# Kernel tuning notes

Hardware: AMD Instinct MI355X
Metric: run time of the kernel (lower is better)

## Reference

```python
import jax, jax.numpy as jnp
import numpy as np


def _cost_volume(image, coords, psize, ksize):
    # image: [c, h, w]; coords: [num, 2] pixel centers; returns [num, psize*psize]
    c, h, w = image.shape
    sp = psize // 2
    pad = ksize // 2 + sp
    ipad = jnp.pad(image, ((0, 0), (pad, pad), (pad, pad)))
    ky = jnp.arange(ksize)
    # top-left corner (in padded coords, before search shift) of each center patch
    rows = coords[:, 0, None, None] + ky[None, :, None]   # [num, k, 1]
    cols = coords[:, 1, None, None] + ky[None, None, :]   # [num, 1, k]
    center = ipad[:, rows + sp, cols + sp]                # [c, num, k, k]
    offs = jnp.stack(jnp.meshgrid(jnp.arange(psize), jnp.arange(psize), indexing='ij'), -1).reshape(-1, 2)

    def ssd(d):
        shifted = ipad[:, rows + d[0], cols + d[1]]       # [c, num, k, k]
        return jnp.sum((shifted - center) ** 2, axis=(0, 2, 3))  # [num]

    vol = jax.lax.map(ssd, offs)                          # [psize*psize, num]
    return vol.T


def _sim_map(image, coords, sigma, psize, ksize):
    c = image.shape[0]
    q = _cost_volume(image, coords, psize, ksize) / (c * ksize * ksize)
    q = jnp.exp(-q / jax.nn.relu(sigma) + 1e-20)          # sigma: [1] broadcasts
    return q[None]                                        # [1, num, psize*psize]


def setup_inputs() -> dict:
    key = jax.random.key(0)
    k1, k2, k3 = jax.random.split(key, 3)
    H = W = 256
    C = 3
    NUM = 2048
    return {
        "img": jax.random.normal(k1, (1, C, H, W), jnp.float32),
        "img_sr": jax.random.normal(k2, (1, C, H, W), jnp.float32),
        "sigma": jnp.array([4.0], jnp.float32),
        "coords": jax.random.randint(k3, (NUM, 2), 0, H),
        "kernel_size_search": 25,
        "kernel_size_center": 9,
    }


def reference(img, img_sr, sigma, coords, kernel_size_search, kernel_size_center):
    s = _sim_map(img[0], coords, sigma, kernel_size_search, kernel_size_center)
    s1 = _sim_map(img_sr[0], coords, sigma, kernel_size_search, kernel_size_center)
    return (s, s1)
```

## Files before the change

kernel.cpp:

```cpp
#include <hip/hip_runtime.h>
#include <hip/hip_fp16.h>

typedef unsigned int uint;
typedef __attribute__((ext_vector_type(2))) _Float16 half2_t;

#define NUM 2048
#define SP 12
#define WIN 33
#define RSTR 20
#define WA_DW (3*WIN*RSTR)
#define HS_STRIDE 14
#define HSE_DW (2*WA_DW)
#define HSO_DW (HSE_DW + WIN*HS_STRIDE)
#define TOT_DW (HSO_DW + WIN*HS_STRIDE)
#define PARTS_DW WA_DW
#define PSTR 8

union U32H2 { uint u; half2_t h; };
__device__ __forceinline__ half2_t uh2(uint u){ U32H2 p; p.u=u; return p.h; }

#if __has_builtin(__builtin_amdgcn_fdot2)
__device__ __forceinline__ float fdot2(uint a, uint b, float c) {
    return __builtin_amdgcn_fdot2(uh2(a), uh2(b), c, false);
}
#else
__device__ __forceinline__ float fdot2(uint a, uint b, float c) {
    half2_t A = uh2(a), B = uh2(b);
    return fmaf((float)A.y, (float)B.y, fmaf((float)A.x, (float)B.x, c));
}
#endif

__device__ __forceinline__ uint packh2(float a, float b) {
    return (uint)__half_as_ushort(__float2half(a)) |
           ((uint)__half_as_ushort(__float2half(b)) << 16);
}

__global__ __launch_bounds__(256, 8) void simmap_kernel(
    const float* __restrict__ img, const float* __restrict__ img_sr,
    const float* __restrict__ sigma, const int* __restrict__ coords,
    float* __restrict__ out)
{
    __shared__ __align__(16) uint lds[TOT_DW];
    __half* wh = (__half*)lds;
    float*  lf = (float*)lds;

    const int n = blockIdx.x;
    const int imgid = blockIdx.y;
    const float* im = imgid ? img_sr : img;
    const int t = threadIdx.x;
    const int w = t >> 6;
    const int l = t & 63;
    const int r0 = coords[2*n];
    const int c0 = coords[2*n+1];

    if (r0 >= 16 && r0 < 240 && c0 >= 16 && c0 < 240) {
        const float* base = im + (r0-16)*256 + (c0-16);
        for (int f = t; f < WIN*WIN; f += 256) {
            int r = f / WIN, x = f - r*WIN;
            int go = r*256 + x;
            #pragma unroll
            for (int c = 0; c < 3; ++c) {
                __half hv = __float2half(base[c*65536 + go]);
                int rowh = (c*WIN + r)*40;
                wh[rowh + x] = hv;
                if (x >= 1)  wh[2*WA_DW + rowh + x - 1] = hv;
                if (x == 32) wh[rowh + 33] = __float2half(0.f);
            }
        }
    } else {
        for (int f = t; f < WIN*WIN; f += 256) {
            int r = f / WIN, x = f - r*WIN;
            int ri = r0 + r - 16, ci = c0 + x - 16;
            bool inb = (ri >= 0 && ri < 256 && ci >= 0 && ci < 256);
            int go = ri*256 + ci;
            #pragma unroll
            for (int c = 0; c < 3; ++c) {
                float v = inb ? im[c*65536 + go] : 0.f;
                __half hv = __float2half(v);
                int rowh = (c*WIN + r)*40;
                wh[rowh + x] = hv;
                if (x >= 1)  wh[2*WA_DW + rowh + x - 1] = hv;
                if (x == 32) wh[rowh + 33] = __float2half(0.f);
            }
        }
    }
    __syncthreads();

    if (w == 0 && l < WIN) {
        float sq[33];
        #pragma unroll
        for (int x = 0; x < 33; ++x) sq[x] = 0.f;
        #pragma unroll 1
        for (int c = 0; c < 3; ++c) {
            const uint* rp = lds + (uint)(c*WIN + l)*RSTR;
            uint U[17];
            { uint4 v = *(const uint4*)(rp);    U[0]=v.x;U[1]=v.y;U[2]=v.z;U[3]=v.w; }
            { uint4 v = *(const uint4*)(rp+4);  U[4]=v.x;U[5]=v.y;U[6]=v.z;U[7]=v.w; }
            { uint4 v = *(const uint4*)(rp+8);  U[8]=v.x;U[9]=v.y;U[10]=v.z;U[11]=v.w; }
            { uint4 v = *(const uint4*)(rp+12); U[12]=v.x;U[13]=v.y;U[14]=v.z;U[15]=v.w; }
            U[16] = rp[16];
            #pragma unroll
            for (int k = 0; k < 17; ++k) {
                half2_t h = uh2(U[k]);
                float x0 = (float)h.x, x1 = (float)h.y;
                sq[2*k] += x0*x0;
                if (2*k + 1 < 33) sq[2*k+1] += x1*x1;
            }
        }
        float s = 0.f;
        #pragma unroll
        for (int j = 0; j < 9; ++j) s += sq[j];
        lf[HSE_DW + l*HS_STRIDE + 0] = s;
        #pragma unroll
        for (int d = 1; d < 25; ++d) {
            s += sq[d+8] - sq[d-1];
            if (d & 1) lf[HSO_DW + l*HS_STRIDE + (d>>1)] = s;
            else       lf[HSE_DW + l*HS_STRIDE + (d>>1)] = s;
        }
    }

    const int lpar = l & 1;
    const int d0e = (l < 50) ? (l >> 1) : 0;
    const uint sbase = lpar ? (uint)WA_DW : 0u;

    float acc[13];
    #pragma unroll
    for (int oo = 0; oo < 13; ++oo) acc[oo] = 0.f;

    const int base  = (w == 0) ? 0 : (w == 1) ? 4 : (w == 2) ? 11 : 19;
    const int nrows = (w == 0) ? 4 : (w == 1) ? 7 : 8;

    #pragma unroll 1
    for (int ridx = base; ridx < base + nrows; ++ridx) {
        const int c = ridx / 9;
        const int i = ridx - 9*c;
        const uint* sp = lds + sbase + (uint)(c*WIN + d0e + i)*RSTR;
        uint S[17];
        { uint4 v = *(const uint4*)(sp);    S[0]=v.x;S[1]=v.y;S[2]=v.z;S[3]=v.w; }
        { uint4 v = *(const uint4*)(sp+4);  S[4]=v.x;S[5]=v.y;S[6]=v.z;S[7]=v.w; }
        { uint4 v = *(const uint4*)(sp+8);  S[8]=v.x;S[9]=v.y;S[10]=v.z;S[11]=v.w; }
        { uint4 v = *(const uint4*)(sp+12); S[12]=v.x;S[13]=v.y;S[14]=v.z;S[15]=v.w; }
        S[16] = sp[16];
        const uint* cp = lds + (uint)(c*WIN + SP + i)*RSTR;
        uint cw[5];
        { uint2 v = *(const uint2*)(cp+6); cw[0]=v.x; cw[1]=v.y; }
        { uint2 v = *(const uint2*)(cp+8); cw[2]=v.x; cw[3]=v.y; }
        cw[4] = cp[10] & 0xFFFFu;
        #pragma unroll
        for (int oo = 0; oo < 13; ++oo) {
            float a = acc[oo];
            #pragma unroll
            for (int jj = 0; jj < 5; ++jj)
                a = fdot2(S[oo + jj], cw[jj], a);
            acc[oo] = a;
        }
    }

    __syncthreads();

    if (l < 50) {
        uint* dst = lds + PARTS_DW + (uint)(w*50 + l)*PSTR;
        uint4 p0, p1;
        p0.x = packh2(acc[0],  acc[1]);  p0.y = packh2(acc[2],  acc[3]);
        p0.z = packh2(acc[4],  acc[5]);  p0.w = packh2(acc[6],  acc[7]);
        p1.x = packh2(acc[8],  acc[9]);  p1.y = packh2(acc[10], acc[11]);
        p1.z = packh2(acc[12], 0.f);     p1.w = 0u;
        ((uint4*)dst)[0] = p0;
        ((uint4*)dst)[1] = p1;
    }
    __syncthreads();

    const int T = 13*w + l;
    if (l >= 13 || T >= 50) return;
    const int d0 = T >> 1;
    const int parity = T & 1;

    float cr[13];
    #pragma unroll
    for (int oo = 0; oo < 13; ++oo) cr[oo] = 0.f;
    #pragma unroll
    for (int ww = 0; ww < 4; ++ww) {
        const uint* src = lds + PARTS_DW + (uint)(ww*50 + T)*PSTR;
        uint4 a = ((const uint4*)src)[0];
        uint4 b = ((const uint4*)src)[1];
        half2_t h;
        h = uh2(a.x); cr[0] += (float)h.x; cr[1] += (float)h.y;
        h = uh2(a.y); cr[2] += (float)h.x; cr[3] += (float)h.y;
        h = uh2(a.z); cr[4] += (float)h.x; cr[5] += (float)h.y;
        h = uh2(a.w); cr[6] += (float)h.x; cr[7] += (float)h.y;
        h = uh2(b.x); cr[8] += (float)h.x; cr[9] += (float)h.y;
        h = uh2(b.y); cr[10] += (float)h.x; cr[11] += (float)h.y;
        h = uh2(b.z); cr[12] += (float)h.x;
    }

    const int hsb = parity ? HSO_DW : HSE_DW;
    float bs[13];
    #pragma unroll
    for (int oo = 0; oo < 13; ++oo) bs[oo] = 0.f;
    #pragma unroll
    for (int i = 0; i < 9; ++i) {
        const float* hr = lf + hsb + (d0 + i)*HS_STRIDE;
        float2 a = *(const float2*)(hr);
        float2 b = *(const float2*)(hr + 2);
        float2 c2 = *(const float2*)(hr + 4);
        float2 d2 = *(const float2*)(hr + 6);
        float2 e2 = *(const float2*)(hr + 8);
        float2 f2 = *(const float2*)(hr + 10);
        bs[0]+=a.x; bs[1]+=a.y; bs[2]+=b.x; bs[3]+=b.y;
        bs[4]+=c2.x; bs[5]+=c2.y; bs[6]+=d2.x; bs[7]+=d2.y;
        bs[8]+=e2.x; bs[9]+=e2.y; bs[10]+=f2.x; bs[11]+=f2.y;
        bs[12]+=hr[12];
    }
    float cc = 0.f;
    #pragma unroll
    for (int i = 0; i < 9; ++i) cc += lf[HSE_DW + (SP + i)*HS_STRIDE + 6];

    const float sg = fmaxf(sigma[0], 0.f);
    const float scl = -1.f / (243.f * sg);
    float* op = out + (size_t)(imgid*NUM + n)*625 + d0*25 + parity;
    #pragma unroll
    for (int oo = 0; oo < 13; ++oo) {
        if (parity && oo == 12) break;
        op[2*oo] = __expf((bs[oo] + cc - 2.f*cr[oo]) * scl + 1e-20f);
    }
}

extern "C" void kernel_launch(void* const* d_in, const int* in_sizes, int n_in,
                              void* d_out, int out_size, void* d_ws, size_t ws_size,
                              hipStream_t stream) {
    const float* img    = (const float*)d_in[0];
    const float* img_sr = (const float*)d_in[1];
    const float* sigma  = (const float*)d_in[2];
    const int*   coords = (const int*)d_in[3];
    float* out = (float*)d_out;
    dim3 grid(NUM, 2);
    simmap_kernel<<<grid, dim3(256), 0, stream>>>(img, img_sr, sigma, coords, out);
}
```

Baseline: 38.96 us.

## Load image rows per thread with packed conversion and precompute vertical box sums

Each of 99 threads now loads one full 33-wide channel row and writes both the even-aligned and odd-shifted half2 rows to LDS with vectorized stores, using packed RTZ conversion, instead of scattered per-element half stores. A running vertical sliding-window sum of the horizontal squared sums is computed by one wave in parallel with the partial-sum write. The final stage then reads precomputed box sums with vector loads rather than summing 9 rows. Launch bounds drop to 6 blocks, and the LDS regions are reassigned so the parts and vertical-sum buffers overlay the staging area.

Result: faster. 35.41 us (-9.1%).

```diff
diff --git a/kernel.cpp b/kernel.cpp
--- a/kernel.cpp
+++ b/kernel.cpp
@@ -3,18 +3,22 @@
 
 typedef unsigned int uint;
 typedef __attribute__((ext_vector_type(2))) _Float16 half2_t;
+typedef __attribute__((ext_vector_type(2))) __fp16 fp16x2_t;
 
 #define NUM 2048
 #define SP 12
 #define WIN 33
 #define RSTR 20
-#define WA_DW (3*WIN*RSTR)
+#define OD_DW (3*WIN*RSTR)
 #define HS_STRIDE 14
-#define HSE_DW (2*WA_DW)
+#define HSE_DW (2*OD_DW)
 #define HSO_DW (HSE_DW + WIN*HS_STRIDE)
 #define TOT_DW (HSO_DW + WIN*HS_STRIDE)
-#define PARTS_DW WA_DW
+#define PARTS_DW 0
 #define PSTR 8
+#define VSE_DW OD_DW
+#define VSO_DW (OD_DW + 400)
+#define VSTR 16
 
 union U32H2 { uint u; half2_t h; };
 __device__ __forceinline__ half2_t uh2(uint u){ U32H2 p; p.u=u; return p.h; }
@@ -35,14 +39,23 @@
            ((uint)__half_as_ushort(__float2half(b)) << 16);
 }
 
-__global__ __launch_bounds__(256, 8) void simmap_kernel(
+#if __has_builtin(__builtin_amdgcn_cvt_pkrtz)
+__device__ __forceinline__ uint pkh2(float a, float b) {
+    union { uint u; fp16x2_t h; } p;
+    p.h = __builtin_amdgcn_cvt_pkrtz(a, b);
+    return p.u;
+}
+#else
+__device__ __forceinline__ uint pkh2(float a, float b) { return packh2(a, b); }
+#endif
+
+__global__ __launch_bounds__(256, 6) void simmap_kernel(
     const float* __restrict__ img, const float* __restrict__ img_sr,
     const float* __restrict__ sigma, const int* __restrict__ coords,
     float* __restrict__ out)
 {
     __shared__ __align__(16) uint lds[TOT_DW];
-    __half* wh = (__half*)lds;
-    float*  lf = (float*)lds;
+    float* lf = (float*)lds;
 
     const int n = blockIdx.x;
     const int imgid = blockIdx.y;
@@ -53,36 +66,51 @@
     const int r0 = coords[2*n];
     const int c0 = coords[2*n+1];
 
-    if (r0 >= 16 && r0 < 240 && c0 >= 16 && c0 < 240) {
-        const float* base = im + (r0-16)*256 + (c0-16);
-        for (int f = t; f < WIN*WIN; f += 256) {
-            int r = f / WIN, x = f - r*WIN;
-            int go = r*256 + x;
-            #pragma unroll
-            for (int c = 0; c < 3; ++c) {
-                __half hv = __float2half(base[c*65536 + go]);
-                int rowh = (c*WIN + r)*40;
-                wh[rowh + x] = hv;
-                if (x >= 1)  wh[2*WA_DW + rowh + x - 1] = hv;
-                if (x == 32) wh[rowh + 33] = __float2half(0.f);
+    if (t < 99) {
+        const int c = t / 33;
+        const int r = t - c*33;
+        const int ri = r0 + r - 16;
+        const float* rowp = im + c*65536 + ri*256 + (c0 - 16);
+        uint Edw[17], Odw[17];
+        if (r0 >= 16 && r0 < 240 && c0 >= 16 && c0 < 240) {
+            float f0 = rowp[0];
+            #pragma unroll
+            for (int k = 0; k < 16; ++k) {
+                float f1 = rowp[2*k+1];
+                float f2 = rowp[2*k+2];
+                Edw[k] = pkh2(f0, f1);
+                Odw[k] = pkh2(f1, f2);
+                f0 = f2;
             }
-        }
-    } else {
-        for (int f = t; f < WIN*WIN; f += 256) {
-            int r = f / WIN, x = f - r*WIN;
-            int ri = r0 + r - 16, ci = c0 + x - 16;
-            bool inb = (ri >= 0 && ri < 256 && ci >= 0 && ci < 256);
-            int go = ri*256 + ci;
-            #pragma unroll
-            for (int c = 0; c < 3; ++c) {
-                float v = inb ? im[c*65536 + go] : 0.f;
-                __half hv = __float2half(v);
-                int rowh = (c*WIN + r)*40;
-                wh[rowh + x] = hv;
-                if (x >= 1)  wh[2*WA_DW + rowh + x - 1] = hv;
-                if (x == 32) wh[rowh + 33] = __float2half(0.f);
+            Edw[16] = pkh2(f0, 0.f);
+            Odw[16] = 0u;
+        } else {
+            const bool rv = ((uint)ri < 256u);
+            float f0 = (rv && (uint)(c0 - 16) < 256u) ? rowp[0] : 0.f;
+            #pragma unroll
+            for (int k = 0; k < 16; ++k) {
+                const int x1 = 2*k + 1, x2 = 2*k + 2;
+                float f1 = (rv && (uint)(c0 - 16 + x1) < 256u) ? rowp[x1] : 0.f;
+                float f2 = (rv && (uint)(c0 - 16 + x2) < 256u) ? rowp[x2] : 0.f;
+                Edw[k] = pkh2(f0, f1);
+                Odw[k] = pkh2(f1, f2);
+                f0 = f2;
             }
-        }
+            Edw[16] = pkh2(f0, 0.f);
+            Odw[16] = 0u;
+        }
+        uint* pE = lds + (uint)t * RSTR;
+        uint* pO = lds + OD_DW + (uint)t * RSTR;
+        ((uint4*)pE)[0] = uint4{Edw[0],Edw[1],Edw[2],Edw[3]};
+        ((uint4*)pE)[1] = uint4{Edw[4],Edw[5],Edw[6],Edw[7]};
+        ((uint4*)pE)[2] = uint4{Edw[8],Edw[9],Edw[10],Edw[11]};
+        ((uint4*)pE)[3] = uint4{Edw[12],Edw[13],Edw[14],Edw[15]};
+        pE[16] = Edw[16];
+        ((uint4*)pO)[0] = uint4{Odw[0],Odw[1],Odw[2],Odw[3]};
+        ((uint4*)pO)[1] = uint4{Odw[4],Odw[5],Odw[6],Odw[7]};
+        ((uint4*)pO)[2] = uint4{Odw[8],Odw[9],Odw[10],Odw[11]};
+        ((uint4*)pO)[3] = uint4{Odw[12],Odw[13],Odw[14],Odw[15]};
+        pO[16] = Odw[16];
     }
     __syncthreads();
 
@@ -121,7 +149,7 @@
 
     const int lpar = l & 1;
     const int d0e = (l < 50) ? (l >> 1) : 0;
-    const uint sbase = lpar ? (uint)WA_DW : 0u;
+    const uint sbase = lpar ? (uint)OD_DW : 0u;
 
     float acc[13];
     #pragma unroll
@@ -168,6 +196,23 @@
         ((uint4*)dst)[0] = p0;
         ((uint4*)dst)[1] = p1;
     }
+    if (w == 1 && l < 25) {
+        const int par = l & 1, col = l >> 1;
+        const int hbase = (par ? HSO_DW : HSE_DW) + col;
+        float f[33];
+        #pragma unroll
+        for (int r = 0; r < 33; ++r) f[r] = lf[hbase + r*HS_STRIDE];
+        float s = 0.f;
+        #pragma unroll
+        for (int i = 0; i < 9; ++i) s += f[i];
+        const int vbase = (par ? VSO_DW : VSE_DW) + col;
+        lf[vbase] = s;
+        #pragma unroll
+        for (int d0 = 1; d0 < 25; ++d0) {
+            s += f[d0+8] - f[d0-1];
+            lf[vbase + d0*VSTR] = s;
+        }
+    }
     __syncthreads();
 
     const int T = 13*w + l;
@@ -193,24 +238,13 @@
         h = uh2(b.z); cr[12] += (float)h.x;
     }
 
-    const int hsb = parity ? HSO_DW : HSE_DW;
-    float bs[13];
-    #pragma unroll
-    for (int oo = 0; oo < 13; ++oo) bs[oo] = 0.f;
-    #pragma unroll
-    for (int i = 0; i < 9; ++i) {
-        const float* hr = lf + hsb + (d0 + i)*HS_STRIDE;
-        float2 a = *(const float2*)(hr);
-        float2 b = *(const float2*)(hr + 2);
-        float2 c2 = *(const float2*)(hr + 4);
-        float2 d2 = *(const float2*)(hr + 6);
-        float2 e2 = *(const float2*)(hr + 8);
-        float2 f2 = *(const float2*)(hr + 10);
-        bs[0]+=a.x; bs[1]+=a.y; bs[2]+=b.x; bs[3]+=b.y;
-        bs[4]+=c2.x; bs[5]+=c2.y; bs[6]+=d2.x; bs[7]+=d2.y;
-        bs[8]+=e2.x; bs[9]+=e2.y; bs[10]+=f2.x; bs[11]+=f2.y;
-        bs[12]+=hr[12];
-    }
+    const float* vr = lf + (parity ? VSO_DW : VSE_DW) + d0*VSTR;
+    float4 v0 = *(const float4*)(vr);
+    float4 v1 = *(const float4*)(vr + 4);
+    float4 v2 = *(const float4*)(vr + 8);
+    float bs[13] = {v0.x,v0.y,v0.z,v0.w,v1.x,v1.y,v1.z,v1.w,
+                    v2.x,v2.y,v2.z,v2.w,vr[12]};
+
     float cc = 0.f;
     #pragma unroll
     for (int i = 0; i < 9; ++i) cc += lf[HSE_DW + (SP + i)*HS_STRIDE + 6];
```
